# Performance work log

Measured on AMD Instinct MI355X. Metric: run time of the kernel, lower is better.

Reference implementation:

```python
import jax, jax.numpy as jnp
import numpy as np

N_HEAD = 16


def setup_inputs() -> dict:
    key = jax.random.key(0)
    ks = jax.random.split(key, 6)
    B, T, C = 8, 1024, 1024
    s = 0.02
    return {
        "x": jax.random.normal(ks[0], (B, T, C), dtype=jnp.float32),
        "Wk": jax.random.normal(ks[1], (C, C), dtype=jnp.float32) * s,
        "bk": jnp.zeros((C,), dtype=jnp.float32),
        "Wq": jax.random.normal(ks[2], (C, C), dtype=jnp.float32) * s,
        "bq": jnp.zeros((C,), dtype=jnp.float32),
        "Wv": jax.random.normal(ks[3], (C, C), dtype=jnp.float32) * s,
        "bv": jnp.zeros((C,), dtype=jnp.float32),
        "Wp": jax.random.normal(ks[4], (C, C), dtype=jnp.float32) * s,
        "bp": jnp.zeros((C,), dtype=jnp.float32),
    }


def reference(x, Wk, bk, Wq, bq, Wv, bv, Wp, bp):
    B, T, C = x.shape
    H = N_HEAD
    d = C // H
    # QKV projections, split heads -> [B, H, T, d]
    k = (x @ Wk + bk).reshape(B, T, H, d).transpose(0, 2, 1, 3)
    q = (x @ Wq + bq).reshape(B, T, H, d).transpose(0, 2, 1, 3)
    v = (x @ Wv + bv).reshape(B, T, H, d).transpose(0, 2, 1, 3)
    # NOTE: original computes K @ Q^T (not Q @ K^T) and scales by C^-0.5
    attn = jnp.einsum('bhid,bhjd->bhij', k, q) * (C ** -0.5)
    mask = jnp.tril(jnp.ones((T, T), dtype=bool))  # tril==0 positions masked
    attn = jnp.where(mask, attn, -jnp.inf)
    attn = jax.nn.softmax(attn, axis=-1)
    out = jnp.einsum('bhij,bhjd->bhid', attn, v)  # [B, H, T, d]
    out = out.transpose(0, 2, 1, 3).reshape(B, T, C)
    return out @ Wp + bp
```

## Files before the change

### kernel.cpp

```cpp
#include <hip/hip_runtime.h>

typedef unsigned short u16;
typedef unsigned int u32;
typedef __bf16 bf16x8 __attribute__((ext_vector_type(8)));
typedef float f32x4 __attribute__((ext_vector_type(4)));

__device__ __forceinline__ u16 f2bf(float f) {
  u32 u = __builtin_bit_cast(u32, f);
  u += 0x7fffu + ((u >> 16) & 1u);
  return (u16)(u >> 16);
}

#define GLOAD_LDS16(g, l) __builtin_amdgcn_global_load_lds( \
    (const __attribute__((address_space(1))) void*)(g),     \
    (__attribute__((address_space(3))) void*)(l), 16, 0, 0)

#define SCK (0.03125f * 1.44269504088896f)

#define BARF() do { asm volatile("" ::: "memory"); \
                    __builtin_amdgcn_s_barrier();  \
                    asm volatile("" ::: "memory"); } while (0)

__global__ __launch_bounds__(256) void prep_k(const float* __restrict__ x,
                                              const float* __restrict__ W0,
                                              const float* __restrict__ W1,
                                              const float* __restrict__ W2,
                                              const float* __restrict__ W3,
                                              u16* __restrict__ xb,
                                              u16* __restrict__ WT) {
  __shared__ float tile[64][65];
  const int tid = threadIdx.x;
  if (blockIdx.x < 4096) {
    size_t i = (size_t)blockIdx.x * 256 + tid;
    const float4* p = reinterpret_cast<const float4*>(x) + i * 2;
    float4 a = p[0], b = p[1];
    u32 w0 = f2bf(a.x) | ((u32)f2bf(a.y) << 16);
    u32 w1 = f2bf(a.z) | ((u32)f2bf(a.w) << 16);
    u32 w2 = f2bf(b.x) | ((u32)f2bf(b.y) << 16);
    u32 w3 = f2bf(b.z) | ((u32)f2bf(b.w) << 16);
    uint4 o; o.x = w0; o.y = w1; o.z = w2; o.w = w3;
    *reinterpret_cast<uint4*>(xb + i * 8) = o;
    return;
  }
  const int bid2 = blockIdx.x - 4096;
  const int z = bid2 >> 8, kt = bid2 & 15, nt = (bid2 >> 4) & 15;
  const float* W = z == 0 ? W0 : z == 1 ? W1 : z == 2 ? W2 : W3;
  u16* dst = WT + (size_t)z * 1024 * 1024;
  const int k0 = kt * 64, n0 = nt * 64;
  const int rr = tid >> 4, c4 = (tid & 15) * 4;
#pragma unroll
  for (int p = 0; p < 4; ++p) {
    int r = rr + p * 16;
    float4 v = *reinterpret_cast<const float4*>(W + (size_t)(k0 + r) * 1024 + n0 + c4);
    tile[r][c4 + 0] = v.x; tile[r][c4 + 1] = v.y;
    tile[r][c4 + 2] = v.z; tile[r][c4 + 3] = v.w;
  }
  __syncthreads();
#pragma unroll
  for (int p = 0; p < 4; ++p) {
    int nl = rr + p * 16;
    u32 w0 = f2bf(tile[c4 + 0][nl]) | ((u32)f2bf(tile[c4 + 1][nl]) << 16);
    u32 w1 = f2bf(tile[c4 + 2][nl]) | ((u32)f2bf(tile[c4 + 3][nl]) << 16);
    uint2 o; o.x = w0; o.y = w1;
    *reinterpret_cast<uint2*>(dst + (size_t)(n0 + nl) * 1024 + k0 + c4) = o;
  }
}

template <int MODE>
__global__ __launch_bounds__(512, 2) void gemm8_k(
    const u16* __restrict__ A, const u16* __restrict__ BT,
    const float* __restrict__ bias0, const float* __restrict__ bias1,
    const float* __restrict__ bias2,
    u16* __restrict__ out_k, u16* __restrict__ out_q, u16* __restrict__ out_vT,
    float* __restrict__ out_f) {
  constexpr int BN = (MODE == 0) ? 192 : 128;
  constexpr int NB = BN / 64;
  constexpr int LPT = 4 + NB;
  constexpr int WCW = BN / 4;
  constexpr int HALF = 8 + NB;

  __shared__ __align__(16) u16 As[2][256 * 64];
  __shared__ __align__(16) u16 Bs[2][BN * 64];

  const int tid = threadIdx.x;
  const int w = tid >> 6, lane = tid & 63;
  const int wr = w >> 2, wc = w & 3;
  const int fr = lane & 15, fq = lane >> 4;
  const int d = fr & 7;

  const int bid = (int)blockIdx.x;
  const int xcd = bid & 7, c = bid >> 3;
  int bx, by;
  if constexpr (MODE == 0) {
    bx = (xcd & 3) * 8 + (c >> 3);
    by = (xcd >> 2) * 8 + (c & 7);
  } else {
    bx = xcd * 4 + (c >> 3);
    by = c & 7;
  }
  const int row0 = bx * 256, col0 = by * BN;

  const int r0 = tid >> 3;
  const int cbg = (tid & 7) ^ (r0 & 7);
  const u16* Asrc = A + (size_t)(row0 + r0) * 1024 + cbg * 8;
  const u16* Bsrc = BT + (size_t)(col0 + r0) * 1024 + cbg * 8;

#define STAGE8(buf, t) do {                                                  \
    _Pragma("unroll")                                                        \
    for (int sw = 0; sw < 4; ++sw)                                           \
      GLOAD_LDS16(Asrc + (size_t)sw * 65536 + (t) * 64,                      \
                  &As[buf][sw * 4096 + tid * 8]);                            \
    _Pragma("unroll")                                                        \
    for (int sw = 0; sw < NB; ++sw)                                          \
      GLOAD_LDS16(Bsrc + (size_t)sw * 65536 + (t) * 64,                      \
                  &Bs[buf][sw * 4096 + tid * 8]);                            \
  } while (0)

#define AOFF(mb, kk) ((wr * 128 + (mb) * 16 + fr) * 128 + (((((kk) << 2) | fq) ^ d) << 4))
#define BOFF(nb, kk) ((wc * WCW + (nb) * 16 + fr) * 128 + (((((kk) << 2) | fq) ^ d) << 4))

  f32x4 acc[8][NB] = {};

  STAGE8(0, 0);
  STAGE8(1, 1);
  asm volatile("s_waitcnt vmcnt(%0)" :: "n"(LPT) : "memory");
  BARF();

#pragma unroll 1
  for (int g = 0; g < 16; ++g) {
    const int buf = g & 1;
    const char* Ac = (const char*)&As[buf][0];
    const char* Bc = (const char*)&Bs[buf][0];
    bf16x8 a[8][2], b[NB][2];

#pragma unroll
    for (int mb = 0; mb < 8; ++mb) a[mb][0] = *(const bf16x8*)(Ac + AOFF(mb, 0));
#pragma unroll
    for (int nb = 0; nb < NB; ++nb) b[nb][0] = *(const bf16x8*)(Bc + BOFF(nb, 0));
#pragma unroll
    for (int mb = 0; mb < 8; ++mb) a[mb][1] = *(const bf16x8*)(Ac + AOFF(mb, 1));
#pragma unroll
    for (int nb = 0; nb < NB; ++nb) b[nb][1] = *(const bf16x8*)(Bc + BOFF(nb, 1));

    asm volatile("s_waitcnt lgkmcnt(%0)" :: "n"(HALF) : "memory");
    __builtin_amdgcn_s_setprio(1);
#pragma unroll
    for (int mb = 0; mb < 8; ++mb)
#pragma unroll
      for (int nb = 0; nb < NB; ++nb)
        acc[mb][nb] = __builtin_amdgcn_mfma_f32_16x16x32_bf16(
            a[mb][0], b[nb][0], acc[mb][nb], 0, 0, 0);
    __builtin_amdgcn_s_setprio(0);

    asm volatile("s_waitcnt lgkmcnt(0)" ::: "memory");
    asm volatile("s_waitcnt vmcnt(0)" ::: "memory");
    BARF();
    if (g + 2 < 16) STAGE8(buf, g + 2);

    __builtin_amdgcn_s_setprio(1);
#pragma unroll
    for (int mb = 0; mb < 8; ++mb)
#pragma unroll
      for (int nb = 0; nb < NB; ++nb)
        acc[mb][nb] = __builtin_amdgcn_mfma_f32_16x16x32_bf16(
            a[mb][1], b[nb][1], acc[mb][nb], 0, 0, 0);
    __builtin_amdgcn_s_setprio(0);
  }
#undef STAGE8
#undef AOFF
#undef BOFF

  if constexpr (MODE == 0) {
#pragma unroll
    for (int mb = 0; mb < 8; ++mb) {
#pragma unroll
      for (int nb = 0; nb < NB; ++nb) {
        const int rg = row0 + wr * 128 + mb * 16 + fq * 4;
        const int cg = col0 + wc * WCW + nb * 16 + fr;
        const int which = cg >> 10;
        const int nloc = cg & 1023;
        const float bv = (which == 0 ? bias0 : which == 1 ? bias1 : bias2)[nloc];
        if (which == 0) {
#pragma unroll
          for (int r = 0; r < 4; ++r)
            out_k[(size_t)(rg + r) * 1024 + nloc] = f2bf((acc[mb][nb][r] + bv) * SCK);
        } else if (which == 1) {
#pragma unroll
          for (int r = 0; r < 4; ++r)
            out_q[(size_t)(rg + r) * 1024 + nloc] = f2bf(acc[mb][nb][r] + bv);
        } else {
          const int bb = rg >> 10, t = rg & 1023;
          const int hh = nloc >> 6, dl = nloc & 63;
          u32 w0 = f2bf(acc[mb][nb][0] + bv) | ((u32)f2bf(acc[mb][nb][1] + bv) << 16);
          u32 w1 = f2bf(acc[mb][nb][2] + bv) | ((u32)f2bf(acc[mb][nb][3] + bv) << 16);
          uint2 ov; ov.x = w0; ov.y = w1;
          *reinterpret_cast<uint2*>(out_vT + ((size_t)(bb * 16 + hh) * 64 + dl) * 1024 + t) = ov;
        }
      }
    }
  } else {
#pragma unroll
    for (int mb = 0; mb < 8; ++mb)
#pragma unroll
      for (int nb = 0; nb < NB; ++nb) {
        const int rg = row0 + wr * 128 + mb * 16 + fq * 4;
        const int cg = col0 + wc * WCW + nb * 16 + fr;
        const float bv = bias0[cg];
#pragma unroll
        for (int r = 0; r < 4; ++r)
          out_f[(size_t)(rg + r) * 1024 + cg] = acc[mb][nb][r] + bv;
      }
  }
}

__global__ __launch_bounds__(256, 2) void projg_k(const u16* __restrict__ A,
                                                  const u16* __restrict__ BT,
                                                  const float* __restrict__ bias,
                                                  float* __restrict__ out_f) {
  __shared__ __align__(16) u16 As[2][128 * 64];
  __shared__ __align__(16) u16 Bs[2][128 * 64];

  const int tid = threadIdx.x;
  const int w = tid >> 6, lane = tid & 63;
  const int wr = w >> 1, wc = w & 1;
  const int fr = lane & 15, fq = lane >> 4;
  const int d = fr & 7;

  const int bid = (int)blockIdx.x;
  const int xcd = bid & 7, c = bid >> 3;
  const int bx = xcd * 8 + (c >> 3);
  const int by = c & 7;
  const int row0 = bx * 128, col0 = by * 128;

  const int r0 = tid >> 3;
  const int cbg = (tid & 7) ^ (r0 & 7);
  const u16* Asrc = A + (size_t)(row0 + r0) * 1024 + cbg * 8;
  const u16* Bsrc = BT + (size_t)(col0 + r0) * 1024 + cbg * 8;

#define STAGEP(buf, t) do {                                                  \
    _Pragma("unroll")                                                        \
    for (int sw = 0; sw < 4; ++sw) {                                         \
      GLOAD_LDS16(Asrc + (size_t)sw * 32768 + (t) * 64,                      \
                  &As[buf][sw * 2048 + tid * 8]);                            \
      GLOAD_LDS16(Bsrc + (size_t)sw * 32768 + (t) * 64,                      \
                  &Bs[buf][sw * 2048 + tid * 8]);                            \
    }                                                                        \
  } while (0)

#define APOFF(mb, kk) ((wr * 64 + (mb) * 16 + fr) * 128 + (((((kk) << 2) | fq) ^ d) << 4))
#define BPOFF(nb, kk) ((wc * 64 + (nb) * 16 + fr) * 128 + (((((kk) << 2) | fq) ^ d) << 4))

  f32x4 acc[4][4] = {};

  STAGEP(0, 0);
  STAGEP(1, 1);
  asm volatile("s_waitcnt vmcnt(8)" ::: "memory");
  BARF();

#pragma unroll 1
  for (int g = 0; g < 16; ++g) {
    const int buf = g & 1;
    const char* Ac = (const char*)&As[buf][0];
    const char* Bc = (const char*)&Bs[buf][0];
    bf16x8 a[4][2], b[4][2];

#pragma unroll
    for (int mb = 0; mb < 4; ++mb) a[mb][0] = *(const bf16x8*)(Ac + APOFF(mb, 0));
#pragma unroll
    for (int nb = 0; nb < 4; ++nb) b[nb][0] = *(const bf16x8*)(Bc + BPOFF(nb, 0));
#pragma unroll
    for (int mb = 0; mb < 4; ++mb) a[mb][1] = *(const bf16x8*)(Ac + APOFF(mb, 1));
#pragma unroll
    for (int nb = 0; nb < 4; ++nb) b[nb][1] = *(const bf16x8*)(Bc + BPOFF(nb, 1));

    asm volatile("s_waitcnt lgkmcnt(8)" ::: "memory");
    __builtin_amdgcn_s_setprio(1);
#pragma unroll
    for (int mb = 0; mb < 4; ++mb)
#pragma unroll
      for (int nb = 0; nb < 4; ++nb)
        acc[mb][nb] = __builtin_amdgcn_mfma_f32_16x16x32_bf16(
            a[mb][0], b[nb][0], acc[mb][nb], 0, 0, 0);
    __builtin_amdgcn_s_setprio(0);

    asm volatile("s_waitcnt lgkmcnt(0)" ::: "memory");
    asm volatile("s_waitcnt vmcnt(0)" ::: "memory");
    BARF();
    if (g + 2 < 16) STAGEP(buf, g + 2);

    __builtin_amdgcn_s_setprio(1);
#pragma unroll
    for (int mb = 0; mb < 4; ++mb)
#pragma unroll
      for (int nb = 0; nb < 4; ++nb)
        acc[mb][nb] = __builtin_amdgcn_mfma_f32_16x16x32_bf16(
            a[mb][1], b[nb][1], acc[mb][nb], 0, 0, 0);
    __builtin_amdgcn_s_setprio(0);
  }
#undef STAGEP
#undef APOFF
#undef BPOFF

#pragma unroll
  for (int mb = 0; mb < 4; ++mb)
#pragma unroll
    for (int nb = 0; nb < 4; ++nb) {
      const int rg = row0 + wr * 64 + mb * 16 + fq * 4;
      const int cg = col0 + wc * 64 + nb * 16 + fr;
      const float bv = bias[cg];
#pragma unroll
      for (int r = 0; r < 4; ++r)
        out_f[(size_t)(rg + r) * 1024 + cg] = acc[mb][nb][r] + bv;
    }
}

__global__ __launch_bounds__(256, 4) void attn_k(const u16* __restrict__ Q,
                                                 const u16* __restrict__ K,
                                                 const u16* __restrict__ vT,
                                                 u16* __restrict__ O) {
  __shared__ __align__(16) u16 KsA[4096], KsB[4096], VsA[4096], VsB[4096];
  __shared__ __align__(16) u16 Plds[4][16][40];
  const int tid = threadIdx.x;
  const int w = tid >> 6, lane = tid & 63;
  const int fr = lane & 15, fq = lane >> 4, koff = fq * 8;

  const int n = blockIdx.x + 8 * (blockIdx.y + 16 * blockIdx.z);
  const int xcd = n & 7, rest = n >> 3;
  const int g = rest >> 3, pair = rest & 7;
  const int hb = xcd + 8 * g;
  const int h = hb & 15, b = hb >> 4;

  const size_t bstride = (size_t)1024 * 1024;
  const u16* Qb = Q + b * bstride + h * 64;
  const u16* Kg = K + b * bstride + h * 64;
  const u16* Vg = vT + ((size_t)(b * 16 + h) * 64) * 1024;

  const int srow = tid >> 3;
  const int scb = (tid & 7) ^ (srow & 7);
  const u16* KgT = Kg + (size_t)srow * 1024 + scb * 8;
  const u16* VgT = Vg + (size_t)srow * 1024 + scb * 8;

  const int vK0 = fr * 128 + ((fq ^ (fr & 7)) << 4);
  const int vK1 = vK0 ^ 64;
  const int pw = w * 1280 + fq * 320 + fr * 2;
  const int pr = w * 1280 + fr * 80 + fq * 16;

#define STAGE(KS, VS, jt) do {                                          \
    GLOAD_LDS16(KgT + (size_t)(jt) * 65536, &KS[tid * 8]);              \
    GLOAD_LDS16(KgT + (size_t)(jt) * 65536 + 32 * 1024, &KS[2048 + tid * 8]); \
    GLOAD_LDS16(VgT + (jt) * 64, &VS[tid * 8]);                         \
    GLOAD_LDS16(VgT + (jt) * 64 + 32 * 1024, &VS[2048 + tid * 8]);      \
  } while (0)

#pragma unroll 1
  for (int ph = 0; ph < 2; ++ph) {
    const int T = ph ? (15 - pair) : pair;
    const int i0 = T * 64;
    const int ibase = i0 + w * 16;

    bf16x8 aq0 = *reinterpret_cast<const bf16x8*>(&Qb[(size_t)(ibase + fr) * 1024 + koff]);
    bf16x8 aq1 = *reinterpret_cast<const bf16x8*>(&Qb[(size_t)(ibase + fr) * 1024 + koff + 32]);

    f32x4 o[4] = {};
    float lp[4] = {0.f, 0.f, 0.f, 0.f};

    auto compute = [&](const u16* KS, const u16* VS, bool diag) {
      const char* Kc = reinterpret_cast<const char*>(KS);
      const char* Vc = reinterpret_cast<const char*>(VS);
      f32x4 s[4];
#pragma unroll
      for (int jc = 0; jc < 4; ++jc) {
        bf16x8 bk0 = *reinterpret_cast<const bf16x8*>(Kc + vK0 + jc * 2048);
        bf16x8 bk1 = *reinterpret_cast<const bf16x8*>(Kc + vK1 + jc * 2048);
        f32x4 z = {};
        z = __builtin_amdgcn_mfma_f32_16x16x32_bf16(aq0, bk0, z, 0, 0, 0);
        s[jc] = __builtin_amdgcn_mfma_f32_16x16x32_bf16(aq1, bk1, z, 0, 0, 0);
      }
      bf16x8 bv0[4], bv1[4];
#pragma unroll
      for (int dn = 0; dn < 4; ++dn) {
        bv0[dn] = *reinterpret_cast<const bf16x8*>(Vc + vK0 + dn * 2048);
        bv1[dn] = *reinterpret_cast<const bf16x8*>(Vc + vK1 + dn * 2048);
      }
      float p[4][4];
      if (diag) {
#pragma unroll
        for (int r = 0; r < 4; ++r) {
          const int il = w * 16 + fq * 4 + r;
#pragma unroll
          for (int jc = 0; jc < 4; ++jc) {
            const int jl = jc * 16 + fr;
            p[jc][r] = (jl <= il) ? __builtin_amdgcn_exp2f(s[jc][r]) : 0.f;
          }
        }
      } else {
#pragma unroll
        for (int r = 0; r < 4; ++r)
#pragma unroll
          for (int jc = 0; jc < 4; ++jc)
            p[jc][r] = __builtin_amdgcn_exp2f(s[jc][r]);
      }
#pragma unroll
      for (int r = 0; r < 4; ++r)
        lp[r] += (p[0][r] + p[1][r]) + (p[2][r] + p[3][r]);
      char* Pc = reinterpret_cast<char*>(&Plds[0][0][0]);
#pragma unroll
      for (int jh = 0; jh < 2; ++jh) {
#pragma unroll
        for (int r = 0; r < 4; ++r)
#pragma unroll
          for (int j2 = 0; j2 < 2; ++j2)
            *reinterpret_cast<u16*>(Pc + pw + r * 80 + j2 * 32) = f2bf(p[jh * 2 + j2][r]);
        bf16x8 ap = *reinterpret_cast<const bf16x8*>(Pc + pr);
#pragma unroll
        for (int dn = 0; dn < 4; ++dn)
          o[dn] = __builtin_amdgcn_mfma_f32_16x16x32_bf16(ap, jh ? bv1[dn] : bv0[dn],
                                                          o[dn], 0, 0, 0);
      }
    };

    STAGE(KsA, VsA, 0);
    int t = 0;
    while (true) {
      {
        const bool more = t < T;
        if (more) STAGE(KsB, VsB, t + 1);
        if (more) { asm volatile("s_waitcnt vmcnt(4)" ::: "memory"); }
        else      { asm volatile("s_waitcnt vmcnt(0)" ::: "memory"); }
        __builtin_amdgcn_s_barrier();
        compute(KsA, VsA, t == T);
        __builtin_amdgcn_s_barrier();
        if (!more) break;
        ++t;
      }
      {
        const bool more = t < T;
        if (more) STAGE(KsA, VsA, t + 1);
        if (more) { asm volatile("s_waitcnt vmcnt(4)" ::: "memory"); }
        else      { asm volatile("s_waitcnt vmcnt(0)" ::: "memory"); }
        __builtin_amdgcn_s_barrier();
        compute(KsB, VsB, t == T);
        __builtin_amdgcn_s_barrier();
        if (!more) break;
        ++t;
      }
    }

#pragma unroll
    for (int x = 1; x < 16; x <<= 1)
#pragma unroll
      for (int r = 0; r < 4; ++r) lp[r] += __shfl_xor(lp[r], x);
#pragma unroll
    for (int r = 0; r < 4; ++r) {
      const float inv = 1.f / lp[r];
      const int ig = ibase + fq * 4 + r;
#pragma unroll
      for (int dn = 0; dn < 4; ++dn)
        O[((size_t)b * 1024 + ig) * 1024 + h * 64 + dn * 16 + fr] = f2bf(o[dn][r] * inv);
    }
  }
#undef STAGE
}

extern "C" void kernel_launch(void* const* d_in, const int* in_sizes, int n_in,
                              void* d_out, int out_size, void* d_ws, size_t ws_size,
                              hipStream_t stream) {
  const float* x  = (const float*)d_in[0];
  const float* Wk = (const float*)d_in[1];
  const float* bk = (const float*)d_in[2];
  const float* Wq = (const float*)d_in[3];
  const float* bq = (const float*)d_in[4];
  const float* Wv = (const float*)d_in[5];
  const float* bv = (const float*)d_in[6];
  const float* Wp = (const float*)d_in[7];
  const float* bp = (const float*)d_in[8];
  float* out = (float*)d_out;

  char* ws = (char*)d_ws;
  u16* xb   = (u16*)(ws);
  u16* WT   = (u16*)(ws + ((size_t)16 << 20));
  u16* kbuf = (u16*)(ws + ((size_t)24 << 20));
  u16* qbuf = (u16*)(ws + ((size_t)40 << 20));
  u16* vT   = (u16*)(ws + ((size_t)56 << 20));
  u16* aout = (u16*)(ws + ((size_t)72 << 20));

  prep_k<<<5120, 256, 0, stream>>>(x, Wk, Wq, Wv, Wp, xb, WT);
  gemm8_k<0><<<512, 512, 0, stream>>>(xb, WT, bk, bq, bv,
                                      kbuf, qbuf, vT, nullptr);
  attn_k<<<dim3(8, 16, 8), 256, 0, stream>>>(kbuf, qbuf, vT, aout);
  projg_k<<<512, 256, 0, stream>>>(aout, WT + (size_t)3 * 1024 * 1024, bp, out);
}
```

Baseline: 128.4 us.

## Process both paired causal query tiles in one shared K/V sweep

Each attention block used to handle its two query tiles (pair and 15-pair) one after the other, staging K/V tiles from global memory separately for each. The phases are now fused: one loop over the longer tile's K/V range computes the long tile every iteration and the short tile while its causal range lasts. Each staged K/V tile therefore serves both query tiles, which cuts global-to-LDS traffic and the number of barrier and pipeline iterations. In exchange it keeps two sets of accumulators and Q fragments live at once, which raises register pressure and could lower occupancy.

```diff
diff --git a/kernel.cpp b/kernel.cpp
--- a/kernel.cpp
+++ b/kernel.cpp
@@ -352,114 +352,123 @@
     GLOAD_LDS16(VgT + (jt) * 64 + 32 * 1024, &VS[2048 + tid * 8]);      \
   } while (0)
 
-#pragma unroll 1
-  for (int ph = 0; ph < 2; ++ph) {
-    const int T = ph ? (15 - pair) : pair;
-    const int i0 = T * 64;
-    const int ibase = i0 + w * 16;
-
-    bf16x8 aq0 = *reinterpret_cast<const bf16x8*>(&Qb[(size_t)(ibase + fr) * 1024 + koff]);
-    bf16x8 aq1 = *reinterpret_cast<const bf16x8*>(&Qb[(size_t)(ibase + fr) * 1024 + koff + 32]);
-
-    f32x4 o[4] = {};
-    float lp[4] = {0.f, 0.f, 0.f, 0.f};
-
-    auto compute = [&](const u16* KS, const u16* VS, bool diag) {
-      const char* Kc = reinterpret_cast<const char*>(KS);
-      const char* Vc = reinterpret_cast<const char*>(VS);
-      f32x4 s[4];
-#pragma unroll
-      for (int jc = 0; jc < 4; ++jc) {
-        bf16x8 bk0 = *reinterpret_cast<const bf16x8*>(Kc + vK0 + jc * 2048);
-        bf16x8 bk1 = *reinterpret_cast<const bf16x8*>(Kc + vK1 + jc * 2048);
-        f32x4 z = {};
-        z = __builtin_amdgcn_mfma_f32_16x16x32_bf16(aq0, bk0, z, 0, 0, 0);
-        s[jc] = __builtin_amdgcn_mfma_f32_16x16x32_bf16(aq1, bk1, z, 0, 0, 0);
+  const int TA = pair, TB = 15 - pair;
+  const int ibA = TA * 64 + w * 16, ibB = TB * 64 + w * 16;
+
+  bf16x8 aqA0 = *reinterpret_cast<const bf16x8*>(&Qb[(size_t)(ibA + fr) * 1024 + koff]);
+  bf16x8 aqA1 = *reinterpret_cast<const bf16x8*>(&Qb[(size_t)(ibA + fr) * 1024 + koff + 32]);
+  bf16x8 aqB0 = *reinterpret_cast<const bf16x8*>(&Qb[(size_t)(ibB + fr) * 1024 + koff]);
+  bf16x8 aqB1 = *reinterpret_cast<const bf16x8*>(&Qb[(size_t)(ibB + fr) * 1024 + koff + 32]);
+
+  f32x4 oA[4] = {}, oB[4] = {};
+  float lpA[4] = {0.f, 0.f, 0.f, 0.f}, lpB[4] = {0.f, 0.f, 0.f, 0.f};
+
+  char* Pc = reinterpret_cast<char*>(&Plds[0][0][0]);
+
+  auto compute = [&](const u16* KS, const u16* VS, bool diag,
+                     bf16x8 aq0, bf16x8 aq1, f32x4* o, float* lp) {
+    const char* Kc = reinterpret_cast<const char*>(KS);
+    const char* Vc = reinterpret_cast<const char*>(VS);
+    f32x4 s[4];
+#pragma unroll
+    for (int jc = 0; jc < 4; ++jc) {
+      bf16x8 bk0 = *reinterpret_cast<const bf16x8*>(Kc + vK0 + jc * 2048);
+      bf16x8 bk1 = *reinterpret_cast<const bf16x8*>(Kc + vK1 + jc * 2048);
+      f32x4 z = {};
+      z = __builtin_amdgcn_mfma_f32_16x16x32_bf16(aq0, bk0, z, 0, 0, 0);
+      s[jc] = __builtin_amdgcn_mfma_f32_16x16x32_bf16(aq1, bk1, z, 0, 0, 0);
+    }
+    bf16x8 bv0[4], bv1[4];
+#pragma unroll
+    for (int dn = 0; dn < 4; ++dn) {
+      bv0[dn] = *reinterpret_cast<const bf16x8*>(Vc + vK0 + dn * 2048);
+      bv1[dn] = *reinterpret_cast<const bf16x8*>(Vc + vK1 + dn * 2048);
+    }
+    float p[4][4];
+    if (diag) {
+#pragma unroll
+      for (int r = 0; r < 4; ++r) {
+        const int il = w * 16 + fq * 4 + r;
+#pragma unroll
+        for (int jc = 0; jc < 4; ++jc) {
+          const int jl = jc * 16 + fr;
+          p[jc][r] = (jl <= il) ? __builtin_amdgcn_exp2f(s[jc][r]) : 0.f;
+        }
       }
-      bf16x8 bv0[4], bv1[4];
-#pragma unroll
-      for (int dn = 0; dn < 4; ++dn) {
-        bv0[dn] = *reinterpret_cast<const bf16x8*>(Vc + vK0 + dn * 2048);
-        bv1[dn] = *reinterpret_cast<const bf16x8*>(Vc + vK1 + dn * 2048);
-      }
-      float p[4][4];
-      if (diag) {
-#pragma unroll
-        for (int r = 0; r < 4; ++r) {
-          const int il = w * 16 + fq * 4 + r;
-#pragma unroll
-          for (int jc = 0; jc < 4; ++jc) {
-            const int jl = jc * 16 + fr;
-            p[jc][r] = (jl <= il) ? __builtin_amdgcn_exp2f(s[jc][r]) : 0.f;
-          }
-        }
-      } else {
-#pragma unroll
-        for (int r = 0; r < 4; ++r)
-#pragma unroll
-          for (int jc = 0; jc < 4; ++jc)
-            p[jc][r] = __builtin_amdgcn_exp2f(s[jc][r]);
-      }
+    } else {
 #pragma unroll
       for (int r = 0; r < 4; ++r)
-        lp[r] += (p[0][r] + p[1][r]) + (p[2][r] + p[3][r]);
-      char* Pc = reinterpret_cast<char*>(&Plds[0][0][0]);
-#pragma unroll
-      for (int jh = 0; jh < 2; ++jh) {
-#pragma unroll
-        for (int r = 0; r < 4; ++r)
-#pragma unroll
-          for (int j2 = 0; j2 < 2; ++j2)
-            *reinterpret_cast<u16*>(Pc + pw + r * 80 + j2 * 32) = f2bf(p[jh * 2 + j2][r]);
-        bf16x8 ap = *reinterpret_cast<const bf16x8*>(Pc + pr);
-#pragma unroll
-        for (int dn = 0; dn < 4; ++dn)
-          o[dn] = __builtin_amdgcn_mfma_f32_16x16x32_bf16(ap, jh ? bv1[dn] : bv0[dn],
-                                                          o[dn], 0, 0, 0);
-      }
-    };
-
-    STAGE(KsA, VsA, 0);
-    int t = 0;
-    while (true) {
-      {
-        const bool more = t < T;
-        if (more) STAGE(KsB, VsB, t + 1);
-        if (more) { asm volatile("s_waitcnt vmcnt(4)" ::: "memory"); }
-        else      { asm volatile("s_waitcnt vmcnt(0)" ::: "memory"); }
-        __builtin_amdgcn_s_barrier();
-        compute(KsA, VsA, t == T);
-        __builtin_amdgcn_s_barrier();
-        if (!more) break;
-        ++t;
-      }
-      {
-        const bool more = t < T;
-        if (more) STAGE(KsA, VsA, t + 1);
-        if (more) { asm volatile("s_waitcnt vmcnt(4)" ::: "memory"); }
-        else      { asm volatile("s_waitcnt vmcnt(0)" ::: "memory"); }
-        __builtin_amdgcn_s_barrier();
-        compute(KsB, VsB, t == T);
-        __builtin_amdgcn_s_barrier();
-        if (!more) break;
-        ++t;
-      }
-    }
-
-#pragma unroll
-    for (int x = 1; x < 16; x <<= 1)
-#pragma unroll
-      for (int r = 0; r < 4; ++r) lp[r] += __shfl_xor(lp[r], x);
+#pragma unroll
+        for (int jc = 0; jc < 4; ++jc)
+          p[jc][r] = __builtin_amdgcn_exp2f(s[jc][r]);
+    }
+#pragma unroll
+    for (int r = 0; r < 4; ++r)
+      lp[r] += (p[0][r] + p[1][r]) + (p[2][r] + p[3][r]);
+#pragma unroll
+    for (int jh = 0; jh < 2; ++jh) {
+#pragma unroll
+      for (int r = 0; r < 4; ++r)
+#pragma unroll
+        for (int j2 = 0; j2 < 2; ++j2)
+          *reinterpret_cast<u16*>(Pc + pw + r * 80 + j2 * 32) = f2bf(p[jh * 2 + j2][r]);
+      bf16x8 ap = *reinterpret_cast<const bf16x8*>(Pc + pr);
+#pragma unroll
+      for (int dn = 0; dn < 4; ++dn)
+        o[dn] = __builtin_amdgcn_mfma_f32_16x16x32_bf16(ap, jh ? bv1[dn] : bv0[dn],
+                                                        o[dn], 0, 0, 0);
+    }
+  };
+
+  STAGE(KsA, VsA, 0);
+  int t = 0;
+  while (true) {
+    {
+      const bool more = t < TB;
+      if (more) STAGE(KsB, VsB, t + 1);
+      if (more) { asm volatile("s_waitcnt vmcnt(4)" ::: "memory"); }
+      else      { asm volatile("s_waitcnt vmcnt(0)" ::: "memory"); }
+      __builtin_amdgcn_s_barrier();
+      compute(KsA, VsA, t == TB, aqB0, aqB1, oB, lpB);
+      if (t <= TA) compute(KsA, VsA, t == TA, aqA0, aqA1, oA, lpA);
+      __builtin_amdgcn_s_barrier();
+      if (!more) break;
+      ++t;
+    }
+    {
+      const bool more = t < TB;
+      if (more) STAGE(KsA, VsA, t + 1);
+      if (more) { asm volatile("s_waitcnt vmcnt(4)" ::: "memory"); }
+      else      { asm volatile("s_waitcnt vmcnt(0)" ::: "memory"); }
+      __builtin_amdgcn_s_barrier();
+      compute(KsB, VsB, t == TB, aqB0, aqB1, oB, lpB);
+      if (t <= TA) compute(KsB, VsB, t == TA, aqA0, aqA1, oA, lpA);
+      __builtin_amdgcn_s_barrier();
+      if (!more) break;
+      ++t;
+    }
+  }
+#undef STAGE
+
+#pragma unroll
+  for (int x = 1; x < 16; x <<= 1)
 #pragma unroll
     for (int r = 0; r < 4; ++r) {
-      const float inv = 1.f / lp[r];
-      const int ig = ibase + fq * 4 + r;
-#pragma unroll
-      for (int dn = 0; dn < 4; ++dn)
-        O[((size_t)b * 1024 + ig) * 1024 + h * 64 + dn * 16 + fr] = f2bf(o[dn][r] * inv);
-    }
-  }
-#undef STAGE
+      lpA[r] += __shfl_xor(lpA[r], x);
+      lpB[r] += __shfl_xor(lpB[r], x);
+    }
+#pragma unroll
+  for (int r = 0; r < 4; ++r) {
+    const float invA = 1.f / lpA[r];
+    const float invB = 1.f / lpB[r];
+    const int igA = ibA + fq * 4 + r;
+    const int igB = ibB + fq * 4 + r;
+#pragma unroll
+    for (int dn = 0; dn < 4; ++dn) {
+      O[((size_t)b * 1024 + igA) * 1024 + h * 64 + dn * 16 + fr] = f2bf(oA[dn][r] * invA);
+      O[((size_t)b * 1024 + igB) * 1024 + h * 64 + dn * 16 + fr] = f2bf(oB[dn][r] * invB);
+    }
+  }
 }
 
 extern "C" void kernel_launch(void* const* d_in, const int* in_sizes, int n_in,
```

New measurement: 287.2 us. 2.24x slower.
